# Performance work log

Measured on AMD Instinct MI355X. Metric: run time of the kernel, lower is better.

The kernel has to match this reference:

```python
import jax, jax.numpy as jnp
from jax import lax
import numpy as np

B, T, H, V, C = 64, 64, 1024, 32000, 10
Z, CD = 32, 8  # latent dim, cond embedding dim


def lstm_scan(x_tbh, h0, c0, Wih, Whh, bih, bhh):
    """PyTorch-convention LSTM over time. x_tbh: [T,B,H]; returns hs [T,B,H]."""
    def step(carry, x):
        h, c = carry
        gates = x @ Wih.T + bih + h @ Whh.T + bhh  # [B,4H]
        i, f, g, o = jnp.split(gates, 4, axis=-1)
        c = jax.nn.sigmoid(f) * c + jax.nn.sigmoid(i) * jnp.tanh(g)
        h = jax.nn.sigmoid(o) * jnp.tanh(c)
        return (h, c), h
    _, hs = lax.scan(step, (h0, c0), x_tbh)
    return hs


def setup_inputs() -> dict:
    key = jax.random.key(0)
    ks = jax.random.split(key, 24)
    s = 0.02
    d = {
        'input_word': jax.random.randint(ks[0], (B, T), 0, V),
        'cond': jax.random.randint(ks[1], (B,), 0, C),
        'emb_N': jax.random.normal(ks[2], (V, H), jnp.float32) * s,
        'Wih_N': jax.random.normal(ks[3], (4 * H, H), jnp.float32) * s,
        'Whh_N': jax.random.normal(ks[4], (4 * H, H), jnp.float32) * s,
        'bih_N': jnp.zeros((4 * H,), jnp.float32),
        'bhh_N': jnp.zeros((4 * H,), jnp.float32),
        'emb_D': jax.random.normal(ks[5], (V, H), jnp.float32) * s,
        'Wih_D': jax.random.normal(ks[6], (4 * H, H), jnp.float32) * s,
        'Whh_D': jax.random.normal(ks[7], (4 * H, H), jnp.float32) * s,
        'bih_D': jnp.zeros((4 * H,), jnp.float32),
        'bhh_D': jnp.zeros((4 * H,), jnp.float32),
        'emb_cond': jax.random.normal(ks[8], (C, CD), jnp.float32) * s,
        'W_mean': jax.random.normal(ks[9], (Z, H), jnp.float32) * s,
        'b_mean': jnp.zeros((Z,), jnp.float32),
        'W_logvar': jax.random.normal(ks[10], (Z, H), jnp.float32) * s,
        'b_logvar': jnp.zeros((Z,), jnp.float32),
        'W_st': jax.random.normal(ks[11], (H, Z + CD), jnp.float32) * s,
        'b_st': jnp.zeros((H,), jnp.float32),
        'W_out': jax.random.normal(ks[12], (V, H), jnp.float32) * s,
        'b_out': jnp.zeros((V,), jnp.float32),
        'eps': jax.random.normal(ks[13], (B, Z), jnp.float32),
    }
    return d


def reference(input_word, cond, emb_N, Wih_N, Whh_N, bih_N, bhh_N,
              emb_D, Wih_D, Whh_D, bih_D, bhh_D, emb_cond,
              W_mean, b_mean, W_logvar, b_logvar, W_st, b_st,
              W_out, b_out, eps):
    cond_e = emb_cond[cond]                              # [B,8]
    # ---- encoder ----
    x_enc = jnp.transpose(emb_N[input_word], (1, 0, 2))  # [T,B,H]
    h0 = jnp.concatenate([jnp.zeros((B, H - CD), x_enc.dtype), cond_e], axis=-1)
    c0 = jnp.zeros((B, H), x_enc.dtype)
    hs = lstm_scan(x_enc, h0, c0, Wih_N, Whh_N, bih_N, bhh_N)
    h_t = hs[-1]                                         # [B,H]
    mean_h = h_t @ W_mean.T + b_mean                     # [B,32]
    logvar_h = h_t @ W_logvar.T + b_logvar               # [B,32]
    latent_h = eps * jnp.exp(0.5 * logvar_h) + mean_h    # reparameterize
    # ---- decoder (teacher forcing, start token 0) ----
    hd0 = jnp.concatenate([latent_h, cond_e], axis=-1) @ W_st.T + b_st  # [B,H]
    cd0 = jnp.zeros((B, H), hd0.dtype)
    dec_tok = jnp.concatenate(
        [jnp.zeros((B, 1), input_word.dtype), input_word[:, :-1]], axis=1)
    x_dec = jnp.transpose(emb_D[dec_tok], (1, 0, 2))     # [T,B,H]
    hs_d = lstm_scan(x_dec, hd0, cd0, Wih_D, Whh_D, bih_D, bhh_D)  # [T,B,H]
    logits = hs_d @ W_out.T + b_out                      # [T,B,V]
    return jnp.transpose(logits, (1, 0, 2))              # [B,T,V]
```

## Files before the change

### kernel.cpp

```cpp
#include <hip/hip_runtime.h>
#include <hip/hip_bf16.h>

typedef unsigned short u16;
typedef unsigned int   u32;
typedef unsigned long long u64;
typedef __attribute__((ext_vector_type(8))) short short8;
typedef __attribute__((ext_vector_type(4))) float f32x4;

#define DEVINL static __device__ __forceinline__

DEVINL u16 f2bf(float x) {
  u32 u = __float_as_uint(x);
  u32 r = (u + 0x7fffu + ((u >> 16) & 1u)) >> 16;
  return (u16)r;
}

#define GLD16(gp, lp) __builtin_amdgcn_global_load_lds(                     \
    (const __attribute__((address_space(1))) u32*)(gp),                     \
    (__attribute__((address_space(3))) u32*)(lp), 16, 0, 0)

__global__ __launch_bounds__(256) void front_all(
    const float* __restrict__ s0, u16* __restrict__ d0,
    const float* __restrict__ s1, u16* __restrict__ d1,
    const float* __restrict__ s2, u16* __restrict__ d2,
    const float* __restrict__ s3, u16* __restrict__ d3,
    const int* __restrict__ cond, const float* __restrict__ emb_cond,
    const float* __restrict__ bihN, const float* __restrict__ bhhN,
    const float* __restrict__ bihD, const float* __restrict__ bhhD,
    float* __restrict__ ce, float* __restrict__ biasN, float* __restrict__ biasD,
    u32* __restrict__ bar,
    const float* __restrict__ embN, const float* __restrict__ embD,
    const int* __restrict__ words, u16* __restrict__ Xe, u16* __restrict__ Xd,
    u16* __restrict__ hb0) {
  int blk = blockIdx.x;
  if (blk < 16384) {
    int p = blk >> 12, local = blk & 4095;
    const float* s = (p == 0) ? s0 : (p == 1) ? s1 : (p == 2) ? s2 : s3;
    u16*         d = (p == 0) ? d0 : (p == 1) ? d1 : (p == 2) ? d2 : d3;
    int i = local * 256 + threadIdx.x;
    float4 v = ((const float4*)s)[i];
    ushort4 o;
    o.x = f2bf(v.x); o.y = f2bf(v.y); o.z = f2bf(v.z); o.w = f2bf(v.w);
    ((ushort4*)d)[i] = o;
  } else if (blk < 16406) {
    int tid = (blk - 16384) * 256 + threadIdx.x;
    if (tid < 512) {
      int b = tid >> 3, j = tid & 7;
      ce[tid] = emb_cond[cond[b] * 8 + j];
    }
    int i = tid - 512;
    if (i >= 0 && i < 4096) {
      biasN[i] = bihN[i] + bhhN[i];
      biasD[i] = bihD[i] + bhhD[i];
    }
    int k = tid - 4608;
    if (k >= 0 && k < 1024) bar[k] = 0;
  } else if (blk < 24598) {
    int dec = (blk >= 20502);
    int r = blk - (dec ? 20502 : 16406);
    int t = r >> 6, b = r & 63;
    int tok = dec ? ((t == 0) ? 0 : words[b * 64 + t - 1]) : words[b * 64 + t];
    const float* emb = dec ? embD : embN;
    u16* X = dec ? Xd : Xe;
    float4 v = ((const float4*)(emb + (size_t)tok * 1024))[threadIdx.x];
    ushort4 o;
    o.x = f2bf(v.x); o.y = f2bf(v.y); o.z = f2bf(v.z); o.w = f2bf(v.w);
    ((ushort4*)(X + (size_t)r * 1024))[threadIdx.x] = o;
  } else {
    int tid = (blk - 24598) * 256 + threadIdx.x;
    int b = tid >> 10, col = tid & 1023;
    float v = (col >= 1016) ? emb_cond[cond[b] * 8 + (col - 1016)] : 0.f;
    hb0[tid] = f2bf(v);
  }
}

__global__ __launch_bounds__(256) void conv_wout(const float* __restrict__ s,
                                                 u16* __restrict__ d) {
  int i = blockIdx.x * 256 + threadIdx.x;
  float4 v = ((const float4*)s)[i];
  ushort4 o;
  o.x = f2bf(v.x); o.y = f2bf(v.y); o.z = f2bf(v.z); o.w = f2bf(v.w);
  ((ushort4*)d)[i] = o;
}

DEVINL void gemm0_body(char* smemc, int bid, int nwg,
                       const u16* __restrict__ A, const u16* __restrict__ B,
                       float* __restrict__ C, const float* __restrict__ bias,
                       int N, int K) {
  u16 (*lA)[256 * 32] = (u16(*)[256 * 32])smemc;
  u16 (*lB)[128 * 32] = (u16(*)[128 * 32])(smemc + 32768);
  const int tid = threadIdx.x;
  const int lane = tid & 63;
  const int wid = tid >> 6;

  const int nn = N >> 7;
  const int wgid = (bid & 7) * (nwg >> 3) + (bid >> 3);
  const int tile_m = (wgid / nn) * 256;
  const int tile_n = (wgid % nn) * 128;
  const int wm = wid >> 1, wn = wid & 1;

  const int ldr = lane >> 2;
  const int lko = (lane & 3) * 8;
  const int l15 = lane & 15;
  const int g4 = lane >> 4;

  const size_t aBase = (size_t)tile_m * K;
  const size_t bBase = (size_t)tile_n * K;

  auto stage = [&](int buf, int k0) {
#pragma unroll
    for (int q = 0; q < 2; ++q) {
      int chk = wid * 2 + q;
      int row = chk * 16 + ldr;
      GLD16(A + aBase + (size_t)row * K + k0 + lko, &lA[buf][chk * 512]);
    }
    int row = wid * 16 + ldr;
    GLD16(B + bBase + (size_t)row * K + k0 + lko, &lB[buf][wid * 512]);
  };

  f32x4 acc[4][4];
#pragma unroll
  for (int i = 0; i < 4; ++i)
#pragma unroll
    for (int j = 0; j < 4; ++j) acc[i][j] = (f32x4)0.f;

  stage(0, 0);
  __syncthreads();

  const int NIT = K >> 5;
  for (int it = 0; it < NIT; ++it) {
    const int cur = it & 1;
    if (it + 1 < NIT) stage(cur ^ 1, (it + 1) * 32);
    short8 af[4], bf[4];
#pragma unroll
    for (int i = 0; i < 4; ++i)
      af[i] = *(const short8*)&lA[cur][(wm * 64 + i * 16 + l15) * 32 + g4 * 8];
#pragma unroll
    for (int j = 0; j < 4; ++j)
      bf[j] = *(const short8*)&lB[cur][(wn * 64 + j * 16 + l15) * 32 + g4 * 8];
#pragma unroll
    for (int i = 0; i < 4; ++i)
#pragma unroll
      for (int j = 0; j < 4; ++j)
        acc[i][j] = __builtin_amdgcn_mfma_f32_16x16x32_bf16(af[i], bf[j], acc[i][j], 0, 0, 0);
    __syncthreads();
  }

#pragma unroll
  for (int i = 0; i < 4; ++i) {
    int row0 = tile_m + wm * 64 + i * 16 + (g4 << 2);
#pragma unroll
    for (int j = 0; j < 4; ++j) {
      int col = tile_n + wn * 64 + j * 16 + l15;
      float bv = bias[col];
#pragma unroll
      for (int e = 0; e < 4; ++e)
        C[(size_t)(row0 + e) * (size_t)N + col] = acc[i][j][e] + bv;
    }
  }
}

DEVINL void lstm_body(char* smemc, const u16* __restrict__ Whh,
                      const float* __restrict__ Xp, u16* __restrict__ hbuf,
                      u16* __restrict__ hs_out, float* __restrict__ hT_out,
                      u32* arrive, u32* prog, int wgi) {
  __builtin_amdgcn_s_setprio(2);
  char* smemA = smemc;
  float (*lg)[16][16] = (float(*)[16][16])(smemc + 32768);
  const int tid = threadIdx.x;
  const int lane = tid & 63;
  const int v = tid >> 6;
  const int gate = v >> 1;
  const int ch = v & 1;
  const int c = wgi >> 5;
  const int j = wgi & 31;
  const int b0 = c * 16, col0 = j * 32;
  const int l15 = lane & 15, g4 = lane >> 4;

  short8 breg[32];
  {
    const u16* Brow = Whh + (size_t)(gate * 1024 + col0 + ch * 16 + l15) * 1024
                          + g4 * 8;
#pragma unroll
    for (int kk = 0; kk < 32; ++kk)
      breg[kk] = *(const short8*)(Brow + kk * 32);
  }

  const int crow = tid >> 5, colw = tid & 31;
  const int bg = b0 + crow, cgl = col0 + colw;
  const int ch2 = colw >> 4, cw = colw & 15;
  float creg = 0.f;

  float xg0, xg1, xg2, xg3;
  {
    size_t xrow = (size_t)bg * 4096 + cgl;
    xg0 = __builtin_nontemporal_load(&Xp[xrow]);
    xg1 = __builtin_nontemporal_load(&Xp[xrow + 1024]);
    xg2 = __builtin_nontemporal_load(&Xp[xrow + 2048]);
    xg3 = __builtin_nontemporal_load(&Xp[xrow + 3072]);
  }

  for (int t = 0; t < 64; ++t) {
    const char* rbase = (const char*)(hbuf + (size_t)(t & 1) * 65536)
                      + (size_t)b0 * 2048;
    u32* wb32 = (u32*)(hbuf + (size_t)((t + 1) & 1) * 65536);

#pragma unroll
    for (int q = 0; q < 4; ++q) {
      int g = q * 512 + tid;
      int row = g >> 7;
      int cb = (g & 127) * 16;
      const u64* src = (const u64*)(rbase + (size_t)row * 2048 + cb);
      u64 lo = __hip_atomic_load(src,     __ATOMIC_RELAXED, __HIP_MEMORY_SCOPE_AGENT);
      u64 hi = __hip_atomic_load(src + 1, __ATOMIC_RELAXED, __HIP_MEMORY_SCOPE_AGENT);
      u64* d = (u64*)(smemA + row * 2048 + (cb ^ ((row & 7) << 4)));
      d[0] = lo; d[1] = hi;
    }
    __syncthreads();

    f32x4 a4[4] = {(f32x4)0.f, (f32x4)0.f, (f32x4)0.f, (f32x4)0.f};
#pragma unroll
    for (int kk = 0; kk < 32; ++kk) {
      int cb2 = kk * 64 + g4 * 16;
      const short8 a = *(const short8*)(smemA + l15 * 2048 + (cb2 ^ ((l15 & 7) << 4)));
      a4[kk & 3] = __builtin_amdgcn_mfma_f32_16x16x32_bf16(a, breg[kk], a4[kk & 3], 0, 0, 0);
    }
    f32x4 asum = a4[0] + a4[1] + a4[2] + a4[3];
    {
      int m = g4 * 4;
#pragma unroll
      for (int e = 0; e < 4; ++e) lg[v][m + e][l15] = asum[e];
    }
    __syncthreads();

    {
      float gi = lg[0 + ch2][crow][cw] + xg0;
      float gf = lg[2 + ch2][crow][cw] + xg1;
      float gg = lg[4 + ch2][crow][cw] + xg2;
      float go = lg[6 + ch2][crow][cw] + xg3;
      float si = 1.f / (1.f + __expf(-gi));
      float sf = 1.f / (1.f + __expf(-gf));
      float so = 1.f / (1.f + __expf(-go));
      float tg = tanhf(gg);
      float cn = sf * creg + si * tg;
      float hn = so * tanhf(cn);
      creg = cn;
      u16 h16 = f2bf(hn);
      u32 mine = h16;
      u32 other = (u32)__shfl_xor((int)mine, 1);
      if (!(colw & 1)) {
        u32 pk = mine | (other << 16);
        __hip_atomic_store(wb32 + (((size_t)bg * 1024 + cgl) >> 1), pk,
                           __ATOMIC_RELAXED, __HIP_MEMORY_SCOPE_AGENT);
        if (hs_out)
          __hip_atomic_store((u32*)hs_out + ((((size_t)t * 64 + bg) * 1024 + cgl) >> 1),
                             pk, __ATOMIC_RELAXED, __HIP_MEMORY_SCOPE_AGENT);
      }
      if (hT_out && t == 63) hT_out[bg * 1024 + cgl] = hn;
    }

    if (t != 63) {
      {
        size_t xrow = (size_t)((t + 1) * 64 + bg) * 4096 + cgl;
        xg0 = __builtin_nontemporal_load(&Xp[xrow]);
        xg1 = __builtin_nontemporal_load(&Xp[xrow + 1024]);
        xg2 = __builtin_nontemporal_load(&Xp[xrow + 2048]);
        xg3 = __builtin_nontemporal_load(&Xp[xrow + 3072]);
      }
      u32 want = (u32)(t + 1);
      asm volatile("s_waitcnt vmcnt(0)" ::: "memory");
      __syncthreads();
      if (tid == 0)
        __hip_atomic_store(&arrive[wgi], want, __ATOMIC_RELAXED,
                           __HIP_MEMORY_SCOPE_AGENT);
      if (tid < 32) {
        int guard = 0;
        while (__hip_atomic_load(&arrive[c * 32 + tid], __ATOMIC_RELAXED,
                                 __HIP_MEMORY_SCOPE_AGENT) < want) {
          __builtin_amdgcn_s_sleep(2);
          if (++guard > (1 << 20)) break;
        }
      }
      __syncthreads();
      if (prog && j == 0 && tid == 0)
        __hip_atomic_store(&prog[c], want, __ATOMIC_RELAXED,
                           __HIP_MEMORY_SCOPE_AGENT);
    }
  }

  if (prog) {
    asm volatile("s_waitcnt vmcnt(0)" ::: "memory");
    __syncthreads();
    if (tid == 0)
      __hip_atomic_store(&arrive[wgi], 64u, __ATOMIC_RELAXED,
                         __HIP_MEMORY_SCOPE_AGENT);
    if (j == 0) {
      if (tid < 32) {
        int guard = 0;
        while (__hip_atomic_load(&arrive[c * 32 + tid], __ATOMIC_RELAXED,
                                 __HIP_MEMORY_SCOPE_AGENT) < 64u) {
          __builtin_amdgcn_s_sleep(2);
          if (++guard > (1 << 20)) break;
        }
      }
      __syncthreads();
      if (tid == 0)
        __hip_atomic_store(&prog[c], 64u, __ATOMIC_RELAXED,
                           __HIP_MEMORY_SCOPE_AGENT);
    }
  }
  __builtin_amdgcn_s_setprio(0);
}

__global__ __launch_bounds__(512, 1) void lstm_cluster(
    const u16* __restrict__ Whh, const float* __restrict__ Xp,
    u16* __restrict__ hbuf, float* __restrict__ hT_out, u32* arrive) {
  __shared__ __align__(16) char smem[40960];
  lstm_body(smem, Whh, Xp, hbuf, nullptr, hT_out, arrive, nullptr, blockIdx.x);
}

__global__ __launch_bounds__(512) void gemm_bt0(
    const u16* __restrict__ A, const u16* __restrict__ B,
    float* __restrict__ C, const float* __restrict__ bias, int N, int K) {
  __shared__ __align__(16) char smem[49152];
  gemm0_body(smem, blockIdx.x, gridDim.x, A, B, C, bias, N, K);
}

__global__ __launch_bounds__(512, 1) void enc_fused(
    const u16* __restrict__ whhN, const float* __restrict__ XpE,
    u16* __restrict__ hbuf, float* __restrict__ hT_out, u32* arrive,
    const u16* __restrict__ Xd, const u16* __restrict__ wihD,
    float* __restrict__ XpD, const float* __restrict__ biasD,
    const float* __restrict__ Wout, u16* __restrict__ wout) {
  __shared__ __align__(16) char smem[49152];
  if (blockIdx.x < 128) {
    lstm_body(smem, whhN, XpE, hbuf, nullptr, hT_out, arrive, nullptr, blockIdx.x);
  } else if (blockIdx.x < 640) {
    gemm0_body(smem, blockIdx.x - 128, 512, Xd, wihD, XpD, biasD, 4096, 1024);
  } else {
    int tid0 = (blockIdx.x - 640) * 512 + threadIdx.x;
    for (int i = tid0; i < 8192000; i += 512 * 512) {
      float4 v = ((const float4*)Wout)[i];
      ushort4 o;
      o.x = f2bf(v.x); o.y = f2bf(v.y); o.z = f2bf(v.z); o.w = f2bf(v.w);
      ((ushort4*)wout)[i] = o;
    }
  }
}

__global__ __launch_bounds__(512, 1) void dec_fused(
    const u16* __restrict__ whhD, const float* __restrict__ XpD,
    u16* __restrict__ hbuf, u16* __restrict__ hsd, u32* arrive, u32* prog,
    const u16* __restrict__ wout, float* __restrict__ out,
    const float* __restrict__ b_out) {
  __shared__ __align__(16) char smem[73728];
  if (blockIdx.x < 128) {
    lstm_body(smem, whhD, XpD, hbuf, hsd, nullptr, arrive, prog, blockIdx.x);
    return;
  }
  u16 (*lA)[256 * 32] = (u16(*)[256 * 32])smem;
  u16 (*lB)[128 * 32] = (u16(*)[128 * 32])(smem + 49152);
  const int tid = threadIdx.x;
  const int lane = tid & 63;
  const int wid = tid >> 6;

  const int i = blockIdx.x - 128;
  const int x = i & 7;
  const int k = i >> 3;
  const int mg = k >> 6;
  const int r  = k & 63;
  const int kn = r >> 1;
  const int mi = r & 1;
  const int tn = kn * 8 + x;
  if (tn >= 250) return;
  const int mt = mg * 2 + mi;
  const int tile_m = mt * 256;
  const int tile_n = tn * 128;
  const int wm = wid >> 1, wn = wid & 1;
  const int N = 32000, K = 1024;

  {
    u32 need = (u32)(mt * 4 + 4);
    if (tid < 4) {
      int guard = 0;
      while (__hip_atomic_load(&prog[tid], __ATOMIC_RELAXED,
                               __HIP_MEMORY_SCOPE_AGENT) < need) {
        __builtin_amdgcn_s_sleep(8);
        if (++guard > (1 << 22)) break;
      }
    }
    __syncthreads();
  }

  const int ldr = lane >> 2;
  const int lko = (lane & 3) * 8;
  const int l15 = lane & 15;
  const int g4 = lane >> 4;

  const size_t aBase = (size_t)tile_m * K;
  const size_t bBase = (size_t)tile_n * K;

  auto stg = [&](int buf, int k0) {
#pragma unroll
    for (int q = 0; q < 2; ++q) {
      int chk = wid * 2 + q;
      int row = chk * 16 + ldr;
      GLD16(hsd + aBase + (size_t)row * K + k0 + lko, &lA[buf][chk * 512]);
    }
    int row = wid * 16 + ldr;
    GLD16(wout + bBase + (size_t)row * K + k0 + lko, &lB[buf][wid * 512]);
  };

  f32x4 acc[4][4];
#pragma unroll
  for (int i2 = 0; i2 < 4; ++i2)
#pragma unroll
    for (int j2 = 0; j2 < 4; ++j2) acc[i2][j2] = (f32x4)0.f;

  stg(0, 0);

  const int NIT = K >> 5;
  for (int it = 0; it < NIT; ++it) {
    const int cur = it % 3;
    if (it + 1 < NIT) {
      stg((it + 1) % 3, (it + 1) * 32);
      asm volatile("s_waitcnt vmcnt(3)" ::: "memory");
    } else {
      asm volatile("s_waitcnt vmcnt(0)" ::: "memory");
    }
    __builtin_amdgcn_s_barrier();
    short8 af[4], bf[4];
#pragma unroll
    for (int i2 = 0; i2 < 4; ++i2)
      af[i2] = *(const short8*)&lA[cur][(wm * 64 + i2 * 16 + l15) * 32 + g4 * 8];
#pragma unroll
    for (int j2 = 0; j2 < 4; ++j2)
      bf[j2] = *(const short8*)&lB[cur][(wn * 64 + j2 * 16 + l15) * 32 + g4 * 8];
#pragma unroll
    for (int i2 = 0; i2 < 4; ++i2)
#pragma unroll
      for (int j2 = 0; j2 < 4; ++j2)
        acc[i2][j2] = __builtin_amdgcn_mfma_f32_16x16x32_bf16(af[i2], bf[j2], acc[i2][j2], 0, 0, 0);
  }

#pragma unroll
  for (int i2 = 0; i2 < 4; ++i2) {
    int row0 = tile_m + wm * 64 + i2 * 16 + (g4 << 2);
#pragma unroll
    for (int j2 = 0; j2 < 4; ++j2) {
      int col = tile_n + wn * 64 + j2 * 16 + l15;
      float bv = b_out[col];
#pragma unroll
      for (int e = 0; e < 4; ++e) {
        int rr = row0 + e;
        size_t o = (size_t)((rr & 63) * 64 + (rr >> 6)) * (size_t)N + col;
        __builtin_nontemporal_store(acc[i2][j2][e] + bv, &out[o]);
      }
    }
  }
}

__global__ __launch_bounds__(256) void latent_hd0_kernel(
    const float* hT, const float* Wm, const float* bm,
    const float* Wl, const float* bl, const float* Wst, const float* bst,
    const float* eps, const float* ce, u16* hb0) {
  __shared__ float red[64][4];
  __shared__ float ml[64];
  __shared__ float lat[40];
  int b = blockIdx.x;
  int tid = threadIdx.x;
  int o = tid >> 2, p = tid & 3;
  const float* w = (o < 32) ? (Wm + (size_t)o * 1024) : (Wl + (size_t)(o - 32) * 1024);
  const float* h = hT + (size_t)b * 1024;
  float s = 0.f;
  for (int k = p * 256; k < p * 256 + 256; ++k) s += h[k] * w[k];
  red[o][p] = s;
  __syncthreads();
  if (tid < 64) {
    float v = red[tid][0] + red[tid][1] + red[tid][2] + red[tid][3];
    v += (tid < 32) ? bm[tid] : bl[tid - 32];
    ml[tid] = v;
  }
  __syncthreads();
  if (tid < 32) lat[tid] = eps[b * 32 + tid] * __expf(0.5f * ml[32 + tid]) + ml[tid];
  if (tid >= 32 && tid < 40) lat[tid] = ce[b * 8 + (tid - 32)];
  __syncthreads();
  for (int hc = tid; hc < 1024; hc += 256) {
    float s2 = bst[hc];
    const float* wr = Wst + (size_t)hc * 40;
#pragma unroll
    for (int j = 0; j < 40; ++j) s2 += lat[j] * wr[j];
    hb0[b * 1024 + hc] = f2bf(s2);
  }
}

extern "C" void kernel_launch(void* const* d_in, const int* in_sizes, int n_in,
                              void* d_out, int out_size, void* d_ws, size_t ws_size,
                              hipStream_t stream) {
  const int*   input_word = (const int*)d_in[0];
  const int*   cond       = (const int*)d_in[1];
  const float* emb_N      = (const float*)d_in[2];
  const float* Wih_N      = (const float*)d_in[3];
  const float* Whh_N      = (const float*)d_in[4];
  const float* bih_N      = (const float*)d_in[5];
  const float* bhh_N      = (const float*)d_in[6];
  const float* emb_D      = (const float*)d_in[7];
  const float* Wih_D      = (const float*)d_in[8];
  const float* Whh_D      = (const float*)d_in[9];
  const float* bih_D      = (const float*)d_in[10];
  const float* bhh_D      = (const float*)d_in[11];
  const float* emb_cond   = (const float*)d_in[12];
  const float* W_mean     = (const float*)d_in[13];
  const float* b_mean     = (const float*)d_in[14];
  const float* W_logvar   = (const float*)d_in[15];
  const float* b_logvar   = (const float*)d_in[16];
  const float* W_st       = (const float*)d_in[17];
  const float* b_st       = (const float*)d_in[18];
  const float* W_out      = (const float*)d_in[19];
  const float* b_out      = (const float*)d_in[20];
  const float* eps        = (const float*)d_in[21];
  float* out = (float*)d_out;

  char* ws = (char*)d_ws;
  size_t off = 0;
  auto alloc = [&](size_t b) { size_t p = off; off += (b + 255) & ~(size_t)255; return p; };
  u16*   wihN = (u16*)(ws + alloc(4096ull * 1024 * 2));
  u16*   whhN = (u16*)(ws + alloc(4096ull * 1024 * 2));
  u16*   wihD = (u16*)(ws + alloc(4096ull * 1024 * 2));
  u16*   whhD = (u16*)(ws + alloc(4096ull * 1024 * 2));
  u16*   wout = (u16*)(ws + alloc(32000ull * 1024 * 2));
  u16*   Xe   = (u16*)(ws + alloc(4096ull * 1024 * 2));
  u16*   Xd   = (u16*)(ws + alloc(4096ull * 1024 * 2));
  float* Xp   = (float*)(ws + alloc(4096ull * 4096 * 4));
  u16*   hsd  = (u16*)(ws + alloc(4096ull * 1024 * 2));
  u16*   hb   = (u16*)(ws + alloc(2ull * 64 * 1024 * 2));
  float* hf   = (float*)(ws + alloc(64ull * 1024 * 4));
  float* biasN = (float*)(ws + alloc(4096 * 4));
  float* biasD = (float*)(ws + alloc(4096 * 4));
  float* ce    = (float*)(ws + alloc(64 * 8 * 4));
  u32*   bar   = (u32*)(ws + alloc(4096));
  size_t base_off = off;
  float* XpD2 = (float*)(ws + alloc(4096ull * 4096 * 4));
  if (base_off > ws_size) return;
  const bool fused = (off <= ws_size);
  float* XpD = fused ? XpD2 : Xp;

  front_all<<<24854, 256, 0, stream>>>(Wih_N, wihN, Whh_N, whhN,
                                       Wih_D, wihD, Whh_D, whhD,
                                       cond, emb_cond,
                                       bih_N, bhh_N, bih_D, bhh_D,
                                       ce, biasN, biasD, bar,
                                       emb_N, emb_D, input_word, Xe, Xd, hb);

  gemm_bt0<<<512, 512, 0, stream>>>(Xe, wihN, Xp, biasN, 4096, 1024);
  if (fused) {
    enc_fused<<<1152, 512, 0, stream>>>(whhN, Xp, hb, hf, bar + 0,
                                        Xd, wihD, XpD, biasD, W_out, wout);
  } else {
    conv_wout<<<32000, 256, 0, stream>>>(W_out, wout);
    lstm_cluster<<<128, 512, 0, stream>>>(whhN, Xp, hb, hf, bar + 0);
  }
  latent_hd0_kernel<<<64, 256, 0, stream>>>(hf, W_mean, b_mean, W_logvar, b_logvar,
                                            W_st, b_st, eps, ce, hb);
  if (!fused)
    gemm_bt0<<<512, 512, 0, stream>>>(Xd, wihD, XpD, biasD, 4096, 1024);
  dec_fused<<<4224, 512, 0, stream>>>(whhD, XpD, hb, hsd, bar + 256, bar + 512,
                                      wout, out, b_out);
}
```

Measured before the change: 940.6 us.

## Fuse encoder input projection GEMM into encoder LSTM kernel with per-tile readiness flags

Drops the separate encoder input-projection GEMM launch and adds 128 producer workgroups inside the fused encoder kernel. Each producer computes 256-row tiles of Xp, stores them nontemporally and bumps a per-tile done counter. The LSTM workgroups wait on that counter before consuming each group of 4 timesteps, so the recurrence can start before the whole projection finishes. The cost is cross-workgroup spin-waiting, which relies on every producer being co-resident. It also adds another workload competing for CUs with the decoder GEMM and weight conversion.

```diff
diff --git a/kernel.cpp b/kernel.cpp
--- a/kernel.cpp
+++ b/kernel.cpp
@@ -160,10 +160,94 @@
   }
 }
 
+DEVINL void xpe_producer(char* smemc, int p,
+                         const u16* __restrict__ Xe, const u16* __restrict__ W,
+                         float* __restrict__ Xp, const float* __restrict__ bias,
+                         u32* __restrict__ done) {
+  u16 (*lA)[256 * 32] = (u16(*)[256 * 32])smemc;
+  u16 (*lB)[128 * 32] = (u16(*)[128 * 32])(smemc + 32768);
+  const int tid = threadIdx.x;
+  const int lane = tid & 63;
+  const int wid = tid >> 6;
+  const int n = p & 31, mq = p >> 5;
+  const int wm = wid >> 1, wn = wid & 1;
+  const int ldr = lane >> 2;
+  const int lko = (lane & 3) * 8;
+  const int l15 = lane & 15;
+  const int g4 = lane >> 4;
+  const int N = 4096, K = 1024;
+  const int tile_n = n * 128;
+  const size_t bBase = (size_t)tile_n * K;
+
+  for (int r2 = 0; r2 < 4; ++r2) {
+    const int mt = r2 * 4 + mq;
+    const int tile_m = mt * 256;
+    const size_t aBase = (size_t)tile_m * K;
+
+    auto stage = [&](int buf, int k0) {
+#pragma unroll
+      for (int q = 0; q < 2; ++q) {
+        int chk = wid * 2 + q;
+        int row = chk * 16 + ldr;
+        GLD16(Xe + aBase + (size_t)row * K + k0 + lko, &lA[buf][chk * 512]);
+      }
+      int row = wid * 16 + ldr;
+      GLD16(W + bBase + (size_t)row * K + k0 + lko, &lB[buf][wid * 512]);
+    };
+
+    f32x4 acc[4][4];
+#pragma unroll
+    for (int i = 0; i < 4; ++i)
+#pragma unroll
+      for (int j = 0; j < 4; ++j) acc[i][j] = (f32x4)0.f;
+
+    stage(0, 0);
+    __syncthreads();
+    const int NIT = K >> 5;
+    for (int it = 0; it < NIT; ++it) {
+      const int cur = it & 1;
+      if (it + 1 < NIT) stage(cur ^ 1, (it + 1) * 32);
+      short8 af[4], bf[4];
+#pragma unroll
+      for (int i = 0; i < 4; ++i)
+        af[i] = *(const short8*)&lA[cur][(wm * 64 + i * 16 + l15) * 32 + g4 * 8];
+#pragma unroll
+      for (int j = 0; j < 4; ++j)
+        bf[j] = *(const short8*)&lB[cur][(wn * 64 + j * 16 + l15) * 32 + g4 * 8];
+#pragma unroll
+      for (int i = 0; i < 4; ++i)
+#pragma unroll
+        for (int j = 0; j < 4; ++j)
+          acc[i][j] = __builtin_amdgcn_mfma_f32_16x16x32_bf16(af[i], bf[j], acc[i][j], 0, 0, 0);
+      __syncthreads();
+    }
+
+#pragma unroll
+    for (int i = 0; i < 4; ++i) {
+      int row0 = tile_m + wm * 64 + i * 16 + (g4 << 2);
+#pragma unroll
+      for (int j = 0; j < 4; ++j) {
+        int col = tile_n + wn * 64 + j * 16 + l15;
+        float bv = bias[col];
+#pragma unroll
+        for (int e = 0; e < 4; ++e)
+          __builtin_nontemporal_store(acc[i][j][e] + bv,
+                                      &Xp[(size_t)(row0 + e) * (size_t)N + col]);
+      }
+    }
+    asm volatile("s_waitcnt vmcnt(0)" ::: "memory");
+    __syncthreads();
+    if (tid == 0)
+      __hip_atomic_fetch_add(&done[mt], 1u, __ATOMIC_RELEASE,
+                             __HIP_MEMORY_SCOPE_AGENT);
+    __syncthreads();
+  }
+}
+
 DEVINL void lstm_body(char* smemc, const u16* __restrict__ Whh,
                       const float* __restrict__ Xp, u16* __restrict__ hbuf,
                       u16* __restrict__ hs_out, float* __restrict__ hT_out,
-                      u32* arrive, u32* prog, int wgi) {
+                      u32* arrive, u32* prog, u32* xpdone, int wgi) {
   __builtin_amdgcn_s_setprio(2);
   char* smemA = smemc;
   float (*lg)[16][16] = (float(*)[16][16])(smemc + 32768);
@@ -191,6 +275,17 @@
   const int ch2 = colw >> 4, cw = colw & 15;
   float creg = 0.f;
 
+  if (xpdone) {
+    if (tid == 0) {
+      int guard = 0;
+      while (__hip_atomic_load(&xpdone[0], __ATOMIC_RELAXED,
+                               __HIP_MEMORY_SCOPE_AGENT) < 32u) {
+        __builtin_amdgcn_s_sleep(2);
+        if (++guard > (1 << 22)) break;
+      }
+    }
+    __syncthreads();
+  }
   float xg0, xg1, xg2, xg3;
   {
     size_t xrow = (size_t)bg * 4096 + cgl;
@@ -260,6 +355,17 @@
     }
 
     if (t != 63) {
+      if (xpdone && (((t + 1) & 3) == 0)) {
+        if (tid == 0) {
+          int guard = 0;
+          while (__hip_atomic_load(&xpdone[(t + 1) >> 2], __ATOMIC_RELAXED,
+                                   __HIP_MEMORY_SCOPE_AGENT) < 32u) {
+            __builtin_amdgcn_s_sleep(2);
+            if (++guard > (1 << 22)) break;
+          }
+        }
+        __syncthreads();
+      }
       {
         size_t xrow = (size_t)((t + 1) * 64 + bg) * 4096 + cgl;
         xg0 = __builtin_nontemporal_load(&Xp[xrow]);
@@ -316,7 +422,8 @@
     const u16* __restrict__ Whh, const float* __restrict__ Xp,
     u16* __restrict__ hbuf, float* __restrict__ hT_out, u32* arrive) {
   __shared__ __align__(16) char smem[40960];
-  lstm_body(smem, Whh, Xp, hbuf, nullptr, hT_out, arrive, nullptr, blockIdx.x);
+  lstm_body(smem, Whh, Xp, hbuf, nullptr, hT_out, arrive, nullptr, nullptr,
+            blockIdx.x);
 }
 
 __global__ __launch_bounds__(512) void gemm_bt0(
@@ -327,18 +434,24 @@
 }
 
 __global__ __launch_bounds__(512, 1) void enc_fused(
-    const u16* __restrict__ whhN, const float* __restrict__ XpE,
+    const u16* __restrict__ whhN, float* __restrict__ XpE,
     u16* __restrict__ hbuf, float* __restrict__ hT_out, u32* arrive,
+    u32* xpdone,
+    const u16* __restrict__ Xe, const u16* __restrict__ wihN,
+    const float* __restrict__ biasN,
     const u16* __restrict__ Xd, const u16* __restrict__ wihD,
     float* __restrict__ XpD, const float* __restrict__ biasD,
     const float* __restrict__ Wout, u16* __restrict__ wout) {
   __shared__ __align__(16) char smem[49152];
   if (blockIdx.x < 128) {
-    lstm_body(smem, whhN, XpE, hbuf, nullptr, hT_out, arrive, nullptr, blockIdx.x);
-  } else if (blockIdx.x < 640) {
-    gemm0_body(smem, blockIdx.x - 128, 512, Xd, wihD, XpD, biasD, 4096, 1024);
+    lstm_body(smem, whhN, XpE, hbuf, nullptr, hT_out, arrive, nullptr, xpdone,
+              blockIdx.x);
+  } else if (blockIdx.x < 256) {
+    xpe_producer(smem, blockIdx.x - 128, Xe, wihN, XpE, biasN, xpdone);
+  } else if (blockIdx.x < 768) {
+    gemm0_body(smem, blockIdx.x - 256, 512, Xd, wihD, XpD, biasD, 4096, 1024);
   } else {
-    int tid0 = (blockIdx.x - 640) * 512 + threadIdx.x;
+    int tid0 = (blockIdx.x - 768) * 512 + threadIdx.x;
     for (int i = tid0; i < 8192000; i += 512 * 512) {
       float4 v = ((const float4*)Wout)[i];
       ushort4 o;
@@ -355,7 +468,8 @@
     const float* __restrict__ b_out) {
   __shared__ __align__(16) char smem[73728];
   if (blockIdx.x < 128) {
-    lstm_body(smem, whhD, XpD, hbuf, hsd, nullptr, arrive, prog, blockIdx.x);
+    lstm_body(smem, whhD, XpD, hbuf, hsd, nullptr, arrive, prog, nullptr,
+              blockIdx.x);
     return;
   }
   u16 (*lA)[256 * 32] = (u16(*)[256 * 32])smem;
@@ -552,11 +666,12 @@
                                        ce, biasN, biasD, bar,
                                        emb_N, emb_D, input_word, Xe, Xd, hb);
 
-  gemm_bt0<<<512, 512, 0, stream>>>(Xe, wihN, Xp, biasN, 4096, 1024);
   if (fused) {
-    enc_fused<<<1152, 512, 0, stream>>>(whhN, Xp, hb, hf, bar + 0,
+    enc_fused<<<1280, 512, 0, stream>>>(whhN, Xp, hb, hf, bar + 0, bar + 768,
+                                        Xe, wihN, biasN,
                                         Xd, wihD, XpD, biasD, W_out, wout);
   } else {
+    gemm_bt0<<<512, 512, 0, stream>>>(Xe, wihN, Xp, biasN, 4096, 1024);
     conv_wout<<<32000, 256, 0, stream>>>(W_out, wout);
     lstm_cluster<<<128, 512, 0, stream>>>(whhN, Xp, hb, hf, bar + 0);
   }
```

Result: no change. 936.6 us (-0.4%).
